# Kernel optimization log

Measured on AMD Instinct MI355X. Metric: run time of the kernel, lower is better.

The kernel has to match this reference:

```python
import jax, jax.numpy as jnp
import numpy as np

EMBED = 768
HEAD = 64
SEQ = 4096
BATCH = 4


def setup_inputs() -> dict:
    key = jax.random.key(0)
    ks = jax.random.split(key, 7)
    s = 1.0 / np.sqrt(EMBED)
    x = jax.random.normal(ks[0], (BATCH, SEQ, EMBED), dtype=jnp.float32)
    Wq = jax.random.uniform(ks[1], (EMBED, HEAD), jnp.float32, -s, s)
    bq = jax.random.uniform(ks[2], (HEAD,), jnp.float32, -s, s)
    Wk = jax.random.uniform(ks[3], (EMBED, HEAD), jnp.float32, -s, s)
    bk = jax.random.uniform(ks[4], (HEAD,), jnp.float32, -s, s)
    Wv = jax.random.uniform(ks[5], (EMBED, HEAD), jnp.float32, -s, s)
    bv = jax.random.uniform(ks[6], (HEAD,), jnp.float32, -s, s)
    return {"x": x, "Wq": Wq, "bq": bq, "Wk": Wk, "bk": bk, "Wv": Wv, "bv": bv}


def reference(x, Wq, bq, Wk, bk, Wv, bv):
    # x: [B,T,E]
    Q = x @ Wq + bq  # [B,T,H]
    K = x @ Wk + bk
    V = x @ Wv + bv
    scale = 1.0 / jnp.sqrt(jnp.asarray(HEAD, dtype=x.dtype))
    wei = jnp.einsum('bqh,bkh->bqk', Q, K) * scale  # [B,T,T]
    T = x.shape[1]
    causal = jnp.tril(jnp.ones((T, T), dtype=bool))
    wei = jnp.where(causal, wei, -jnp.inf)
    wei = jax.nn.softmax(wei, axis=-1)
    return jnp.einsum('bqk,bkh->bqh', wei, V)  # [B,T,H]
```

## Files before the change

kernel.cpp:

```cpp
#include <hip/hip_runtime.h>


#define BB 4
#define TT 4096
#define EE 768
#define HH 64
#define BT (BB*TT)

typedef __attribute__((ext_vector_type(8))) short short8;
typedef __attribute__((ext_vector_type(4))) float f32x4;
#define MFMA16(a,b,c) __builtin_amdgcn_mfma_f32_16x16x32_bf16(a,b,c,0,0,0)
#define QSCALE 0.18033688011112042f

static __device__ __forceinline__ float bflo(unsigned a){ return __uint_as_float(a << 16); }
static __device__ __forceinline__ unsigned short f2bf(float f){
    unsigned x = __float_as_uint(f);
    x += 0x7fffu + ((x >> 16) & 1u);
    return (unsigned short)(x >> 16);
}
template<int FP32>
static __device__ __forceinline__ float ldin(const void* p, int idx){
    if (FP32) return ((const float*)p)[idx];
    return bflo(((const unsigned short*)p)[idx]);
}

__global__ __launch_bounds__(256) void probe_kernel(const unsigned short* x, int* flag){
    __shared__ int cnt;
    if (threadIdx.x == 0) cnt = 0;
    __syncthreads();
    int c = 0;
    #pragma unroll
    for (int i = 0; i < 16; i++){
        unsigned u = x[threadIdx.x * 16 + i];
        unsigned e = (u >> 7) & 0xFFu;
        if (e >= 140u) c++;
    }
    atomicAdd(&cnt, c);
    __syncthreads();
    if (threadIdx.x == 0) *flag = (cnt > 32) ? 1 : 0;
}

template<int FP32>
static __device__ void wt_body(const void* W, int wi, int e0, unsigned short* wt){
    __shared__ unsigned short ts[64 * 72];
    const int tid = threadIdx.x;
    #pragma unroll
    for (int p = 0; p < 2; p++){
        int i = p * 256 + tid;
        int r = i >> 3, g = i & 7;
        unsigned short v[8];
        if (FP32){
            const float* src = (const float*)W + (size_t)(e0 + r) * HH + g * 8;
            const float4 a = *(const float4*)src, b = *(const float4*)(src + 4);
            v[0]=f2bf(a.x); v[1]=f2bf(a.y); v[2]=f2bf(a.z); v[3]=f2bf(a.w);
            v[4]=f2bf(b.x); v[5]=f2bf(b.y); v[6]=f2bf(b.z); v[7]=f2bf(b.w);
        } else {
            const unsigned short* src = (const unsigned short*)W + (size_t)(e0 + r) * HH + g * 8;
            #pragma unroll
            for (int j = 0; j < 8; j++) v[j] = src[j];
        }
        #pragma unroll
        for (int j = 0; j < 8; j++) ts[r * 72 + g * 8 + j] = v[j];
    }
    __syncthreads();
    #pragma unroll
    for (int p = 0; p < 2; p++){
        int i = p * 256 + tid;
        int h = i >> 3, g = i & 7;
        unsigned short v[8];
        #pragma unroll
        for (int j = 0; j < 8; j++) v[j] = ts[(g * 8 + j) * 72 + h];
        unsigned short* dst = wt + (size_t)(wi * 64 + h) * EE + e0 + g * 8;
        uint4 pk;
        pk.x = (unsigned)v[0] | ((unsigned)v[1] << 16);
        pk.y = (unsigned)v[2] | ((unsigned)v[3] << 16);
        pk.z = (unsigned)v[4] | ((unsigned)v[5] << 16);
        pk.w = (unsigned)v[6] | ((unsigned)v[7] << 16);
        *(uint4*)dst = pk;
    }
}
__global__ __launch_bounds__(256) void wt_kernel(
    const void* Wq, const void* Wk, const void* Wv, unsigned short* wt, const int* flag){
    const int wi = blockIdx.x / 12;
    const int e0 = (blockIdx.x % 12) * 64;
    const void* W = (wi == 0) ? Wq : (wi == 1) ? Wk : Wv;
    if (*flag) wt_body<1>(W, wi, e0, wt);
    else       wt_body<0>(W, wi, e0, wt);
}

template<int FP32>
static __device__ void qkv_body(const void* x, const unsigned short* wt,
    const void* bq, const void* bk, const void* bv,
    unsigned short* Qw, unsigned short* Kw, unsigned short* VTw,
    unsigned short* xs, unsigned short* wsl)
{
    const int tid = threadIdx.x, lane = tid & 63, w = tid >> 6;
    const int l15 = lane & 15, quad = lane >> 4;
    const int m0 = blockIdx.x * 32;
    const int rh = (w & 1) * 16;
    const int ng = (w >> 1) * 6;

    f32x4 acc[6];
    #pragma unroll
    for (int i = 0; i < 6; i++) acc[i] = (f32x4)(0.f);

    const int srow = tid >> 3, sg = tid & 7;

    for (int c = 0; c < 12; c++){
        const int c0 = c * 64;
        __syncthreads();
        {
            short8 v;
            if (FP32){
                const float* src = (const float*)x + (size_t)(m0 + srow) * EE + c0 + sg * 8;
                const float4 a = *(const float4*)src, b2 = *(const float4*)(src + 4);
                v[0]=(short)f2bf(a.x); v[1]=(short)f2bf(a.y); v[2]=(short)f2bf(a.z); v[3]=(short)f2bf(a.w);
                v[4]=(short)f2bf(b2.x); v[5]=(short)f2bf(b2.y); v[6]=(short)f2bf(b2.z); v[7]=(short)f2bf(b2.w);
            } else {
                v = *(const short8*)((const unsigned short*)x + (size_t)(m0 + srow) * EE + c0 + sg * 8);
            }
            *(short8*)&xs[srow * 72 + sg * 8] = v;
        }
        #pragma unroll
        for (int p = 0; p < 6; p++){
            int i = p * 256 + tid;
            int n = i >> 3, g2 = i & 7;
            *(short8*)&wsl[n * 72 + g2 * 8] = *(const short8*)(wt + (size_t)n * EE + c0 + g2 * 8);
        }
        __syncthreads();
        #pragma unroll
        for (int kst = 0; kst < 2; kst++){
            const short8 a = *(const short8*)&xs[(rh + l15) * 72 + kst * 32 + quad * 8];
            #pragma unroll
            for (int nf = 0; nf < 6; nf++){
                const short8 bfr = *(const short8*)&wsl[((ng + nf) * 16 + l15) * 72 + kst * 32 + quad * 8];
                acc[nf] = MFMA16(a, bfr, acc[nf]);
            }
        }
    }
    #pragma unroll
    for (int nf = 0; nf < 6; nf++){
        const int gi = ng + nf;
        const int wi = gi >> 2;
        const int h = (gi & 3) * 16 + l15;
        const void* bp = (wi == 0) ? bq : (wi == 1) ? bk : bv;
        const float bias = ldin<FP32>(bp, h);
        if (wi == 0){
            #pragma unroll
            for (int rr = 0; rr < 4; rr++){
                const int tok = m0 + rh + quad * 4 + rr;
                Qw[(size_t)tok * HH + h] = f2bf((acc[nf][rr] + bias) * QSCALE);
            }
        } else if (wi == 1){
            #pragma unroll
            for (int rr = 0; rr < 4; rr++){
                const int tok = m0 + rh + quad * 4 + rr;
                Kw[(size_t)tok * HH + h] = f2bf(acc[nf][rr] + bias);
            }
        } else {
            const int tok0 = m0 + rh + quad * 4;
            const int bloc = tok0 >> 12;
            const int tl = tok0 & 4095;
            uint2 pk;
            pk.x = (unsigned)f2bf(acc[nf][0] + bias) | ((unsigned)f2bf(acc[nf][1] + bias) << 16);
            pk.y = (unsigned)f2bf(acc[nf][2] + bias) | ((unsigned)f2bf(acc[nf][3] + bias) << 16);
            *(uint2*)&VTw[(size_t)(bloc * 64 + h) * TT + tl] = pk;
        }
    }
}
__global__ __launch_bounds__(256) void qkv_kernel(
    const void* x, const unsigned short* wt,
    const void* bq, const void* bk, const void* bv,
    unsigned short* Qw, unsigned short* Kw, unsigned short* VTw, const int* flag){
    __shared__ unsigned short xs[32 * 72];
    __shared__ unsigned short wsl[192 * 72];
    if (*flag) qkv_body<1>(x, wt, bq, bk, bv, Qw, Kw, VTw, xs, wsl);
    else       qkv_body<0>(x, wt, bq, bk, bv, Qw, Kw, VTw, xs, wsl);
}

__global__ __launch_bounds__(512, 2) void attn_kernel(
    const unsigned short* __restrict__ Q,
    const unsigned short* __restrict__ K, const unsigned short* __restrict__ VT,
    void* __restrict__ out, const int* __restrict__ flag)
{
    __shared__ unsigned short Pl[8][1152];
    __shared__ unsigned short Opart[8][32][68];
    __shared__ float lpart[8][32];

    const int mode = *flag;
    const int z = blockIdx.x;
    const int b = z & 3;
    const int pair = z >> 2;
    const int tid = threadIdx.x;
    const int lane = tid & 63;
    const int w = tid >> 6;
    const int l15 = lane & 15, quad = lane >> 4;
    const int brow = b * TT;

    for (int phase = 0; phase < 2; phase++){
        const int qt = phase ? (127 - pair) : pair;
        const int q0 = qt * 32;
        const int nkb = (qt >> 1) + 1;

        f32x4 O[2][4];
        float lsum[2][4];
        #pragma unroll
        for (int mt = 0; mt < 2; mt++)
            #pragma unroll
            for (int i = 0; i < 4; i++){ O[mt][i] = (f32x4)(0.f); lsum[mt][i] = 0.f; }

        if (w < nkb){
            short8 qf[2][2];
            #pragma unroll
            for (int mt = 0; mt < 2; mt++)
                #pragma unroll
                for (int kst = 0; kst < 2; kst++)
                    qf[mt][kst] = *(const short8*)(Q + (size_t)(brow + q0 + mt * 16 + l15) * HH + kst * 32 + quad * 8);

            short8 kf[4][2];
            #pragma unroll
            for (int c = 0; c < 4; c++)
                #pragma unroll
                for (int kst = 0; kst < 2; kst++)
                    kf[c][kst] = *(const short8*)(K + (size_t)(brow + w * 64 + c * 16 + l15) * HH + kst * 32 + quad * 8);

            for (int u = w; u < nkb; u += 8){
                const int k0 = u * 64;
                f32x4 sacc[2][4];
                #pragma unroll
                for (int mt = 0; mt < 2; mt++)
                    #pragma unroll
                    for (int c = 0; c < 4; c++){
                        sacc[mt][c] = (f32x4)(0.f);
                        sacc[mt][c] = MFMA16(qf[mt][0], kf[c][0], sacc[mt][c]);
                        sacc[mt][c] = MFMA16(qf[mt][1], kf[c][1], sacc[mt][c]);
                    }
                short8 vf[4][2];
                #pragma unroll
                for (int c = 0; c < 4; c++)
                    #pragma unroll
                    for (int kst = 0; kst < 2; kst++)
                        vf[c][kst] = *(const short8*)(VT + (size_t)(b * 64 + c * 16 + l15) * TT + k0 + kst * 32 + quad * 8);
                if (u + 8 < nkb){
                    const int kn0 = (u + 8) * 64;
                    #pragma unroll
                    for (int c = 0; c < 4; c++)
                        #pragma unroll
                        for (int kst = 0; kst < 2; kst++)
                            kf[c][kst] = *(const short8*)(K + (size_t)(brow + kn0 + c * 16 + l15) * HH + kst * 32 + quad * 8);
                }
                const bool diag = (u == nkb - 1);
                #pragma unroll
                for (int mt = 0; mt < 2; mt++){
                    #pragma unroll
                    for (int c = 0; c < 4; c++){
                        #pragma unroll
                        for (int rr = 0; rr < 4; rr++){
                            float sv = sacc[mt][c][rr];
                            if (diag){
                                const int kg = k0 + c * 16 + l15;
                                const int qg = q0 + mt * 16 + quad * 4 + rr;
                                sv = (kg <= qg) ? sv : -1e30f;
                            }
                            const float p = exp2f(sv);
                            lsum[mt][rr] += p;
                            Pl[w][(quad * 4 + rr) * 72 + c * 16 + l15] = f2bf(p);
                        }
                    }
                    const short8 pf0 = *(const short8*)&Pl[w][l15 * 72 + quad * 8];
                    const short8 pf1 = *(const short8*)&Pl[w][l15 * 72 + 32 + quad * 8];
                    #pragma unroll
                    for (int c2 = 0; c2 < 4; c2++){
                        O[mt][c2] = MFMA16(pf0, vf[c2][0], O[mt][c2]);
                        O[mt][c2] = MFMA16(pf1, vf[c2][1], O[mt][c2]);
                    }
                }
            }
            #pragma unroll
            for (int mt = 0; mt < 2; mt++)
                #pragma unroll
                for (int rr = 0; rr < 4; rr++){
                    #pragma unroll
                    for (int off = 1; off < 16; off <<= 1)
                        lsum[mt][rr] += __shfl_xor(lsum[mt][rr], off, 64);
                }
        }
        #pragma unroll
        for (int mt = 0; mt < 2; mt++)
            #pragma unroll
            for (int rr = 0; rr < 4; rr++){
                const int row = mt * 16 + quad * 4 + rr;
                #pragma unroll
                for (int c2 = 0; c2 < 4; c2++)
                    Opart[w][row][c2 * 16 + l15] = f2bf(O[mt][c2][rr]);
                if (l15 == 0) lpart[w][row] = lsum[mt][rr];
            }
        __syncthreads();
        #pragma unroll
        for (int i = 0; i < 4; i++){
            const int e = i * 512 + tid;
            const int r = e >> 6, h = e & 63;
            float num = 0.f, den = 0.f;
            #pragma unroll
            for (int ww = 0; ww < 8; ww++){
                num += bflo(Opart[ww][r][h]);
                den += lpart[ww][r];
            }
            const float ov = num / den;
            const size_t gi = (size_t)(brow + q0 + r) * HH + h;
            if (mode) ((float*)out)[gi] = ov;
            else      ((unsigned short*)out)[gi] = f2bf(ov);
        }
        __syncthreads();
    }
}

extern "C" void kernel_launch(void* const* d_in, const int* in_sizes, int n_in,
                              void* d_out, int out_size, void* d_ws, size_t ws_size,
                              hipStream_t stream) {
    const void* x  = d_in[0];
    const void* Wq = d_in[1];
    const void* bq = d_in[2];
    const void* Wk = d_in[3];
    const void* bk = d_in[4];
    const void* Wv = d_in[5];
    const void* bv = d_in[6];

    unsigned short* Qw  = (unsigned short*)d_ws;
    unsigned short* Kw  = Qw + (size_t)BT * HH;
    unsigned short* VTw = Kw + (size_t)BT * HH;
    unsigned short* wt  = VTw + (size_t)BT * HH;
    int* flag  = (int*)(wt + (size_t)192 * EE);

    probe_kernel<<<1, 256, 0, stream>>>((const unsigned short*)x, flag);
    wt_kernel<<<36, 256, 0, stream>>>(Wq, Wk, Wv, wt, flag);
    qkv_kernel<<<512, 256, 0, stream>>>(x, wt, bq, bk, bv, Qw, Kw, VTw, flag);
    attn_kernel<<<256, 512, 0, stream>>>(Qw, Kw, VTw, d_out, flag);
}
```

Measured before the change: 166.8 us.

## Fold dtype probe into weight transpose, split QKV columns, one q-tile per attention block

Moves the input dtype probe into the weight-transpose kernel, which removes one launch. The QKV projection is split into two column halves, doubling the grid to 1024 blocks with smaller shared memory and an occupancy hint. The attention kernel drops its paired two-phase loop, so each block handles one 32-row query tile. The grid doubles to 512 blocks and launch bounds target 4 blocks per CU, with shared buffers merged to reduce LDS. This trades the causal load-balancing pairing for more parallelism and occupancy, relying on the hardware scheduler, with heavy tiles launched first.

```diff
diff --git a/kernel.cpp b/kernel.cpp
--- a/kernel.cpp
+++ b/kernel.cpp
@@ -22,22 +22,6 @@
 static __device__ __forceinline__ float ldin(const void* p, int idx){
     if (FP32) return ((const float*)p)[idx];
     return bflo(((const unsigned short*)p)[idx]);
-}
-
-__global__ __launch_bounds__(256) void probe_kernel(const unsigned short* x, int* flag){
-    __shared__ int cnt;
-    if (threadIdx.x == 0) cnt = 0;
-    __syncthreads();
-    int c = 0;
-    #pragma unroll
-    for (int i = 0; i < 16; i++){
-        unsigned u = x[threadIdx.x * 16 + i];
-        unsigned e = (u >> 7) & 0xFFu;
-        if (e >= 140u) c++;
-    }
-    atomicAdd(&cnt, c);
-    __syncthreads();
-    if (threadIdx.x == 0) *flag = (cnt > 32) ? 1 : 0;
 }
 
 template<int FP32>
@@ -80,12 +64,28 @@
     }
 }
 __global__ __launch_bounds__(256) void wt_kernel(
-    const void* Wq, const void* Wk, const void* Wv, unsigned short* wt, const int* flag){
+    const unsigned short* xu, const void* Wq, const void* Wk, const void* Wv,
+    unsigned short* wt, int* flag){
+    __shared__ int cnt;
+    const int tid = threadIdx.x;
+    if (tid == 0) cnt = 0;
+    __syncthreads();
+    int c = 0;
+    #pragma unroll
+    for (int i = 0; i < 16; i++){
+        unsigned u = xu[tid * 16 + i];
+        unsigned e = (u >> 7) & 0xFFu;
+        if (e >= 140u) c++;
+    }
+    atomicAdd(&cnt, c);
+    __syncthreads();
+    const int fp32 = (cnt > 32) ? 1 : 0;
+    if (blockIdx.x == 0 && tid == 0) *flag = fp32;
     const int wi = blockIdx.x / 12;
     const int e0 = (blockIdx.x % 12) * 64;
     const void* W = (wi == 0) ? Wq : (wi == 1) ? Wk : Wv;
-    if (*flag) wt_body<1>(W, wi, e0, wt);
-    else       wt_body<0>(W, wi, e0, wt);
+    if (fp32) wt_body<1>(W, wi, e0, wt);
+    else      wt_body<0>(W, wi, e0, wt);
 }
 
 template<int FP32>
@@ -96,13 +96,15 @@
 {
     const int tid = threadIdx.x, lane = tid & 63, w = tid >> 6;
     const int l15 = lane & 15, quad = lane >> 4;
-    const int m0 = blockIdx.x * 32;
+    const int z = blockIdx.x;
+    const int m0 = (z >> 1) * 32;
+    const int nh = z & 1;
     const int rh = (w & 1) * 16;
-    const int ng = (w >> 1) * 6;
-
-    f32x4 acc[6];
-    #pragma unroll
-    for (int i = 0; i < 6; i++) acc[i] = (f32x4)(0.f);
+    const int ngl = (w >> 1) * 3;
+
+    f32x4 acc[3];
+    #pragma unroll
+    for (int i = 0; i < 3; i++) acc[i] = (f32x4)(0.f);
 
     const int srow = tid >> 3, sg = tid & 7;
 
@@ -122,25 +124,26 @@
             *(short8*)&xs[srow * 72 + sg * 8] = v;
         }
         #pragma unroll
-        for (int p = 0; p < 6; p++){
+        for (int p = 0; p < 3; p++){
             int i = p * 256 + tid;
             int n = i >> 3, g2 = i & 7;
-            *(short8*)&wsl[n * 72 + g2 * 8] = *(const short8*)(wt + (size_t)n * EE + c0 + g2 * 8);
+            *(short8*)&wsl[n * 72 + g2 * 8] =
+                *(const short8*)(wt + (size_t)(nh * 96 + n) * EE + c0 + g2 * 8);
         }
         __syncthreads();
         #pragma unroll
         for (int kst = 0; kst < 2; kst++){
             const short8 a = *(const short8*)&xs[(rh + l15) * 72 + kst * 32 + quad * 8];
             #pragma unroll
-            for (int nf = 0; nf < 6; nf++){
-                const short8 bfr = *(const short8*)&wsl[((ng + nf) * 16 + l15) * 72 + kst * 32 + quad * 8];
+            for (int nf = 0; nf < 3; nf++){
+                const short8 bfr = *(const short8*)&wsl[((ngl + nf) * 16 + l15) * 72 + kst * 32 + quad * 8];
                 acc[nf] = MFMA16(a, bfr, acc[nf]);
             }
         }
     }
     #pragma unroll
-    for (int nf = 0; nf < 6; nf++){
-        const int gi = ng + nf;
+    for (int nf = 0; nf < 3; nf++){
+        const int gi = nh * 6 + ngl + nf;
         const int wi = gi >> 2;
         const int h = (gi & 3) * 16 + l15;
         const void* bp = (wi == 0) ? bq : (wi == 1) ? bk : bv;
@@ -168,150 +171,147 @@
         }
     }
 }
-__global__ __launch_bounds__(256) void qkv_kernel(
+__global__ __launch_bounds__(256, 4) void qkv_kernel(
     const void* x, const unsigned short* wt,
     const void* bq, const void* bk, const void* bv,
     unsigned short* Qw, unsigned short* Kw, unsigned short* VTw, const int* flag){
     __shared__ unsigned short xs[32 * 72];
-    __shared__ unsigned short wsl[192 * 72];
+    __shared__ unsigned short wsl[96 * 72];
     if (*flag) qkv_body<1>(x, wt, bq, bk, bv, Qw, Kw, VTw, xs, wsl);
     else       qkv_body<0>(x, wt, bq, bk, bv, Qw, Kw, VTw, xs, wsl);
 }
 
-__global__ __launch_bounds__(512, 2) void attn_kernel(
+__global__ __launch_bounds__(512, 4) void attn_kernel(
     const unsigned short* __restrict__ Q,
     const unsigned short* __restrict__ K, const unsigned short* __restrict__ VT,
     void* __restrict__ out, const int* __restrict__ flag)
 {
-    __shared__ unsigned short Pl[8][1152];
-    __shared__ unsigned short Opart[8][32][68];
+    __shared__ unsigned short sbuf[8][2304];
     __shared__ float lpart[8][32];
 
     const int mode = *flag;
     const int z = blockIdx.x;
     const int b = z & 3;
-    const int pair = z >> 2;
+    const int qt = 127 - (z >> 2);
+    const int q0 = qt * 32;
+    const int nkb = (qt >> 1) + 1;
     const int tid = threadIdx.x;
     const int lane = tid & 63;
     const int w = tid >> 6;
     const int l15 = lane & 15, quad = lane >> 4;
     const int brow = b * TT;
 
-    for (int phase = 0; phase < 2; phase++){
-        const int qt = phase ? (127 - pair) : pair;
-        const int q0 = qt * 32;
-        const int nkb = (qt >> 1) + 1;
-
-        f32x4 O[2][4];
-        float lsum[2][4];
+    f32x4 O[2][4];
+    float lsum[2][4];
+    #pragma unroll
+    for (int mt = 0; mt < 2; mt++)
+        #pragma unroll
+        for (int i = 0; i < 4; i++){ O[mt][i] = (f32x4)(0.f); lsum[mt][i] = 0.f; }
+
+    if (w < nkb){
+        short8 qf[2][2];
         #pragma unroll
         for (int mt = 0; mt < 2; mt++)
             #pragma unroll
-            for (int i = 0; i < 4; i++){ O[mt][i] = (f32x4)(0.f); lsum[mt][i] = 0.f; }
-
-        if (w < nkb){
-            short8 qf[2][2];
+            for (int kst = 0; kst < 2; kst++)
+                qf[mt][kst] = *(const short8*)(Q + (size_t)(brow + q0 + mt * 16 + l15) * HH + kst * 32 + quad * 8);
+
+        short8 kf[4][2];
+        #pragma unroll
+        for (int c = 0; c < 4; c++)
+            #pragma unroll
+            for (int kst = 0; kst < 2; kst++)
+                kf[c][kst] = *(const short8*)(K + (size_t)(brow + w * 64 + c * 16 + l15) * HH + kst * 32 + quad * 8);
+
+        for (int u = w; u < nkb; u += 8){
+            const int k0 = u * 64;
+            f32x4 sacc[2][4];
             #pragma unroll
             for (int mt = 0; mt < 2; mt++)
                 #pragma unroll
+                for (int c = 0; c < 4; c++){
+                    sacc[mt][c] = (f32x4)(0.f);
+                    sacc[mt][c] = MFMA16(qf[mt][0], kf[c][0], sacc[mt][c]);
+                    sacc[mt][c] = MFMA16(qf[mt][1], kf[c][1], sacc[mt][c]);
+                }
+            short8 vf[4][2];
+            #pragma unroll
+            for (int c = 0; c < 4; c++)
+                #pragma unroll
                 for (int kst = 0; kst < 2; kst++)
-                    qf[mt][kst] = *(const short8*)(Q + (size_t)(brow + q0 + mt * 16 + l15) * HH + kst * 32 + quad * 8);
-
-            short8 kf[4][2];
-            #pragma unroll
-            for (int c = 0; c < 4; c++)
-                #pragma unroll
-                for (int kst = 0; kst < 2; kst++)
-                    kf[c][kst] = *(const short8*)(K + (size_t)(brow + w * 64 + c * 16 + l15) * HH + kst * 32 + quad * 8);
-
-            for (int u = w; u < nkb; u += 8){
-                const int k0 = u * 64;
-                f32x4 sacc[2][4];
-                #pragma unroll
-                for (int mt = 0; mt < 2; mt++)
-                    #pragma unroll
-                    for (int c = 0; c < 4; c++){
-                        sacc[mt][c] = (f32x4)(0.f);
-                        sacc[mt][c] = MFMA16(qf[mt][0], kf[c][0], sacc[mt][c]);
-                        sacc[mt][c] = MFMA16(qf[mt][1], kf[c][1], sacc[mt][c]);
-                    }
-                short8 vf[4][2];
+                    vf[c][kst] = *(const short8*)(VT + (size_t)(b * 64 + c * 16 + l15) * TT + k0 + kst * 32 + quad * 8);
+            if (u + 8 < nkb){
+                const int kn0 = (u + 8) * 64;
                 #pragma unroll
                 for (int c = 0; c < 4; c++)
                     #pragma unroll
                     for (int kst = 0; kst < 2; kst++)
-                        vf[c][kst] = *(const short8*)(VT + (size_t)(b * 64 + c * 16 + l15) * TT + k0 + kst * 32 + quad * 8);
-                if (u + 8 < nkb){
-                    const int kn0 = (u + 8) * 64;
+                        kf[c][kst] = *(const short8*)(K + (size_t)(brow + kn0 + c * 16 + l15) * HH + kst * 32 + quad * 8);
+            }
+            const bool diag = (u == nkb - 1);
+            #pragma unroll
+            for (int mt = 0; mt < 2; mt++){
+                #pragma unroll
+                for (int c = 0; c < 4; c++){
                     #pragma unroll
-                    for (int c = 0; c < 4; c++)
-                        #pragma unroll
-                        for (int kst = 0; kst < 2; kst++)
-                            kf[c][kst] = *(const short8*)(K + (size_t)(brow + kn0 + c * 16 + l15) * HH + kst * 32 + quad * 8);
-                }
-                const bool diag = (u == nkb - 1);
-                #pragma unroll
-                for (int mt = 0; mt < 2; mt++){
-                    #pragma unroll
-                    for (int c = 0; c < 4; c++){
-                        #pragma unroll
-                        for (int rr = 0; rr < 4; rr++){
-                            float sv = sacc[mt][c][rr];
-                            if (diag){
-                                const int kg = k0 + c * 16 + l15;
-                                const int qg = q0 + mt * 16 + quad * 4 + rr;
-                                sv = (kg <= qg) ? sv : -1e30f;
-                            }
-                            const float p = exp2f(sv);
-                            lsum[mt][rr] += p;
-                            Pl[w][(quad * 4 + rr) * 72 + c * 16 + l15] = f2bf(p);
+                    for (int rr = 0; rr < 4; rr++){
+                        float sv = sacc[mt][c][rr];
+                        if (diag){
+                            const int kg = k0 + c * 16 + l15;
+                            const int qg = q0 + mt * 16 + quad * 4 + rr;
+                            sv = (kg <= qg) ? sv : -1e30f;
                         }
-                    }
-                    const short8 pf0 = *(const short8*)&Pl[w][l15 * 72 + quad * 8];
-                    const short8 pf1 = *(const short8*)&Pl[w][l15 * 72 + 32 + quad * 8];
-                    #pragma unroll
-                    for (int c2 = 0; c2 < 4; c2++){
-                        O[mt][c2] = MFMA16(pf0, vf[c2][0], O[mt][c2]);
-                        O[mt][c2] = MFMA16(pf1, vf[c2][1], O[mt][c2]);
+                        const float p = exp2f(sv);
+                        lsum[mt][rr] += p;
+                        sbuf[w][mt * 1152 + (quad * 4 + rr) * 72 + c * 16 + l15] = f2bf(p);
                     }
                 }
             }
             #pragma unroll
-            for (int mt = 0; mt < 2; mt++)
-                #pragma unroll
-                for (int rr = 0; rr < 4; rr++){
-                    #pragma unroll
-                    for (int off = 1; off < 16; off <<= 1)
-                        lsum[mt][rr] += __shfl_xor(lsum[mt][rr], off, 64);
+            for (int mt = 0; mt < 2; mt++){
+                const short8 pf0 = *(const short8*)&sbuf[w][mt * 1152 + l15 * 72 + quad * 8];
+                const short8 pf1 = *(const short8*)&sbuf[w][mt * 1152 + l15 * 72 + 32 + quad * 8];
+                #pragma unroll
+                for (int c2 = 0; c2 < 4; c2++){
+                    O[mt][c2] = MFMA16(pf0, vf[c2][0], O[mt][c2]);
+                    O[mt][c2] = MFMA16(pf1, vf[c2][1], O[mt][c2]);
                 }
+            }
         }
         #pragma unroll
         for (int mt = 0; mt < 2; mt++)
             #pragma unroll
             for (int rr = 0; rr < 4; rr++){
-                const int row = mt * 16 + quad * 4 + rr;
-                #pragma unroll
-                for (int c2 = 0; c2 < 4; c2++)
-                    Opart[w][row][c2 * 16 + l15] = f2bf(O[mt][c2][rr]);
-                if (l15 == 0) lpart[w][row] = lsum[mt][rr];
-            }
-        __syncthreads();
-        #pragma unroll
-        for (int i = 0; i < 4; i++){
-            const int e = i * 512 + tid;
-            const int r = e >> 6, h = e & 63;
-            float num = 0.f, den = 0.f;
-            #pragma unroll
-            for (int ww = 0; ww < 8; ww++){
-                num += bflo(Opart[ww][r][h]);
-                den += lpart[ww][r];
-            }
-            const float ov = num / den;
-            const size_t gi = (size_t)(brow + q0 + r) * HH + h;
-            if (mode) ((float*)out)[gi] = ov;
-            else      ((unsigned short*)out)[gi] = f2bf(ov);
-        }
-        __syncthreads();
+                #pragma unroll
+                for (int off = 1; off < 16; off <<= 1)
+                    lsum[mt][rr] += __shfl_xor(lsum[mt][rr], off, 64);
+            }
+    }
+    #pragma unroll
+    for (int mt = 0; mt < 2; mt++)
+        #pragma unroll
+        for (int rr = 0; rr < 4; rr++){
+            const int row = mt * 16 + quad * 4 + rr;
+            #pragma unroll
+            for (int c2 = 0; c2 < 4; c2++)
+                sbuf[w][row * 72 + c2 * 16 + l15] = f2bf(O[mt][c2][rr]);
+            if (l15 == 0) lpart[w][row] = lsum[mt][rr];
+        }
+    __syncthreads();
+    #pragma unroll
+    for (int i = 0; i < 4; i++){
+        const int e = i * 512 + tid;
+        const int r = e >> 6, h = e & 63;
+        float num = 0.f, den = 0.f;
+        #pragma unroll
+        for (int ww = 0; ww < 8; ww++){
+            num += bflo(sbuf[ww][r * 72 + h]);
+            den += lpart[ww][r];
+        }
+        const float ov = num / den;
+        const size_t gi = (size_t)(brow + q0 + r) * HH + h;
+        if (mode) ((float*)out)[gi] = ov;
+        else      ((unsigned short*)out)[gi] = f2bf(ov);
     }
 }
 
@@ -332,8 +332,7 @@
     unsigned short* wt  = VTw + (size_t)BT * HH;
     int* flag  = (int*)(wt + (size_t)192 * EE);
 
-    probe_kernel<<<1, 256, 0, stream>>>((const unsigned short*)x, flag);
-    wt_kernel<<<36, 256, 0, stream>>>(Wq, Wk, Wv, wt, flag);
-    qkv_kernel<<<512, 256, 0, stream>>>(x, wt, bq, bk, bv, Qw, Kw, VTw, flag);
-    attn_kernel<<<256, 512, 0, stream>>>(Qw, Kw, VTw, d_out, flag);
-}
+    wt_kernel<<<36, 256, 0, stream>>>((const unsigned short*)x, Wq, Wk, Wv, wt, flag);
+    qkv_kernel<<<1024, 256, 0, stream>>>(x, wt, bq, bk, bv, Qw, Kw, VTw, flag);
+    attn_kernel<<<512, 512, 0, stream>>>(Qw, Kw, VTw, d_out, flag);
+}
```

Measured after the change: 228.5 us. +37.0%, slower.
